# Kernel optimization log

Measured on AMD Instinct MI355X. Metric: run time of the kernel, lower is better.

## Reference

```python
import jax, jax.numpy as jnp
import numpy as np
from jax import lax

HIDDEN = 512
EPS = 1e-5


def _conv(x, w):
    # NCHW conv, 3x3, SAME padding, no bias (padding = kernel_size // 2 == 1)
    return lax.conv_general_dilated(
        x, w, window_strides=(1, 1), padding='SAME',
        dimension_numbers=('NCHW', 'OIHW', 'NCHW'))


def setup_inputs() -> dict:
    key = jax.random.key(0)
    ks = jax.random.split(key, 5)
    N, C, H, W = 32, HIDDEN, 32, 32
    fan = C * 9
    std = float(1.0 / np.sqrt(fan))
    return {
        'x': jax.random.normal(ks[0], (N, C, H, W), jnp.float32),
        'w_q': jax.random.normal(ks[1], (C, C, 3, 3), jnp.float32) * std,
        'w_k': jax.random.normal(ks[2], (C, C, 3, 3), jnp.float32) * std,
        'w_v': jax.random.normal(ks[3], (C, C, 3, 3), jnp.float32) * std,
        'w_o': jax.random.normal(ks[4], (C, C, 3, 3), jnp.float32) * std,
        'gamma': jnp.ones((C,), jnp.float32),
        'beta': jnp.zeros((C,), jnp.float32),
    }


def reference(x, w_q, w_k, w_v, w_o, gamma, beta):
    C = x.shape[1]
    q = _conv(x, w_q)  # [N,C,H,W]
    k = _conv(x, w_k)
    v = _conv(x, w_v)
    # (query.unsqueeze(1) * key.unsqueeze(0)).sum(2) == channel contraction
    att = jnp.einsum('ichw,jchw->ijhw', q, k) / jnp.sqrt(jnp.asarray(C, x.dtype))
    att = jax.nn.softmax(att, axis=1)  # softmax over key instances
    virt = jnp.einsum('ijhw,jchw->ichw', att, v)  # [N,C,H,W]
    # GroupNorm(1, C): normalize over (C,H,W) per instance, per-channel affine
    mean = jnp.mean(virt, axis=(1, 2, 3), keepdims=True)
    var = jnp.var(virt, axis=(1, 2, 3), keepdims=True)
    virt = (virt - mean) * lax.rsqrt(var + EPS)
    virt = virt * gamma[None, :, None, None] + beta[None, :, None, None]
    virt = jax.nn.relu(virt)
    virt = _conv(virt, w_o)
    # Dropout(0.2) is identity in eval mode
    return x + virt
```

## Files before the change

kernel.cpp:

```cpp
#include <hip/hip_runtime.h>

namespace {

constexpr int kN  = 32;
constexpr int kC  = 512;
constexpr int kH  = 32;
constexpr int kW  = 32;
constexpr int kHW = kH * kW;

constexpr int PCH   = 36992;
constexpr size_t WTF_ELEMS = (size_t)9 * kC * kC;
constexpr size_t XH_ELEMS  = (size_t)kN * 16 * PCH;
constexpr size_t QKV_ELEMS = (size_t)kN * kHW * kC;

using bf16x8 = __attribute__((ext_vector_type(8))) short;
using bf16x4 = __attribute__((ext_vector_type(4))) short;
using f32x4  = __attribute__((ext_vector_type(4))) float;

__device__ __forceinline__ float bf2f(short s) {
  unsigned u = ((unsigned)(unsigned short)s) << 16;
  return __builtin_bit_cast(float, u);
}
__device__ __forceinline__ short f2bf(float f) {
  unsigned u = __builtin_bit_cast(unsigned, f);
  u += 0x7FFFu + ((u >> 16) & 1u);
  return (short)(u >> 16);
}
__device__ __forceinline__ void gload_lds16(const void* g, void* l) {
  __builtin_amdgcn_global_load_lds(
      (const __attribute__((address_space(1))) void*)g,
      (__attribute__((address_space(3))) void*)l, 16, 0, 0);
}

__global__ __launch_bounds__(256) void wtf_pack_kernel(
    const float* __restrict__ w, short* __restrict__ wtf) {
  __shared__ float tile[32][289];
  const int co0 = blockIdx.x * 32;
  const int ci0 = blockIdx.y * 32;
  for (int idx = threadIdx.x; idx < 32 * 288; idx += 256) {
    int c = idx % 288, r = idx / 288;
    tile[r][c] = w[(size_t)(co0 + r) * (kC * 9) + (size_t)ci0 * 9 + c];
  }
  __syncthreads();
  const int kkb  = ci0 >> 5;
  const int nnG0 = co0 >> 4;
  for (int g = threadIdx.x; g < 9 * 2 * 64; g += 256) {
    int laneg = g & 63;
    int nnL   = (g >> 6) & 1;
    int t     = g >> 7;
    int hi    = laneg >> 4;
    int coL   = nnL * 16 + (laneg & 15);
    bf16x8 pk;
#pragma unroll
    for (int j = 0; j < 8; ++j) pk[j] = f2bf(tile[coL][(hi * 8 + j) * 9 + t]);
    *(bf16x8*)&wtf[(((size_t)t * 16 + kkb) * 32 + nnG0 + nnL) * 512 + laneg * 8] = pk;
  }
}

__global__ __launch_bounds__(256) void x2xh_kernel(
    const float* __restrict__ x, short* __restrict__ xh) {
  __shared__ float tile[32][33];
  const int ch = blockIdx.x;
  const int h  = blockIdx.y;
  const int n  = blockIdx.z;
  const int w0 = threadIdx.x & 31;
  const int c0 = threadIdx.x >> 5;
#pragma unroll
  for (int pass = 0; pass < 4; ++pass) {
    int cir = pass * 8 + c0;
    tile[w0][cir] = x[(((size_t)n * kC + ch * 32 + cir) * kH + h) * kW + w0];
  }
  __syncthreads();
  const int wv = threadIdx.x >> 3;
  const int g4 = (threadIdx.x & 7) * 4;
  bf16x4 pk;
#pragma unroll
  for (int j = 0; j < 4; ++j) pk[j] = f2bf(tile[wv][g4 + j]);
  *(bf16x4*)&xh[(((size_t)n * 16 + ch) * 1156 + (size_t)(h + 1) * 34 + (wv + 1)) * 32 + g4] = pk;
}

__global__ __launch_bounds__(256, 2) void conv_qkv_kernel(
    const short* __restrict__ xin,
    const short* __restrict__ wtq, const short* __restrict__ wtk,
    const short* __restrict__ wtv,
    short* __restrict__ outq, short* __restrict__ outk,
    short* __restrict__ outv) {
  __shared__ __align__(16) short As[3][8192];
  const int tid  = threadIdx.x;
  const int lane = tid & 63;
  const int l15  = lane & 15, lhi = lane >> 4;
  const int wv   = tid >> 6;
  const int wm   = wv >> 1, wn = wv & 1;
  const int wbase = tid & 192;

  const int xcd = blockIdx.x & 7;
  const int m   = blockIdx.x >> 3;
  const int co0 = (m >> 5) * 64;
  const int spt = m & 7;
  const int n   = xcd * 4 + ((m >> 3) & 3);
  const int h0  = spt * 4;
  const int sp0 = spt * 128;

  const short* srcA = xin + (size_t)n * (16 * PCH) + (size_t)h0 * (34 * 32);
  const size_t boff = ((size_t)(co0 >> 4) + wn * 2) * 512 + lane * 8;
  const short* bp[3] = {wtq + boff, wtk + boff, wtv + boff};

  f32x4 acc[3][4][2];
#pragma unroll
  for (int c = 0; c < 3; ++c)
#pragma unroll
    for (int mf = 0; mf < 4; ++mf)
#pragma unroll
      for (int nf = 0; nf < 2; ++nf)
#pragma unroll
        for (int r = 0; r < 4; ++r) acc[c][mf][nf][r] = 0.f;

#define STAGE_A(kk, buf)                                                      \
  {                                                                           \
    const short* gA = srcA + (size_t)(kk) * PCH;                              \
    _Pragma("unroll") for (int pass = 0; pass < 4; ++pass)                    \
        gload_lds16(gA + (size_t)(pass * 256 + tid) * 8,                      \
                    &As[buf][(pass * 256 + wbase) * 8]);                      \
  }

  STAGE_A(0, 0);
  STAGE_A(1, 1);
  bf16x8 cur[6], nxt[6];
#pragma unroll
  for (int j = 0; j < 6; ++j)
    cur[j] = *(const bf16x8*)&bp[j >> 1][(size_t)(j & 1) * 512];

  int ab = 0;
  int sb = 2;
  for (int kk = 0; kk < 16; ++kk) {
    asm volatile("s_waitcnt vmcnt(10)" ::: "memory");
    __builtin_amdgcn_s_barrier();
#pragma unroll
    for (int t = 0; t < 9; ++t) {
      {
        const int nt  = (t < 8) ? (t + 1) : 0;
        const int nkk = (t < 8) ? kk : kk + 1;
        const size_t bo = (size_t)(nt * 16 + nkk) * 16384;
#pragma unroll
        for (int j = 0; j < 6; ++j)
          nxt[j] = *(const bf16x8*)&bp[j >> 1][bo + (size_t)(j & 1) * 512];
      }
      if (t == 1 && kk < 14) STAGE_A(kk + 2, sb);
      const int dy = t / 3, dx = t % 3;
      bf16x8 a[4];
#pragma unroll
      for (int mf = 0; mf < 4; ++mf) {
        const int pb = (wm * 2 + (mf >> 1) + dy) * 34 + (mf & 1) * 16 + l15 + dx;
        a[mf] = *(const bf16x8*)&As[ab][pb * 32 + lhi * 8];
      }
      __builtin_amdgcn_s_setprio(1);
#pragma unroll
      for (int c = 0; c < 3; ++c)
#pragma unroll
        for (int mf = 0; mf < 4; ++mf)
#pragma unroll
          for (int nf = 0; nf < 2; ++nf)
            acc[c][mf][nf] = __builtin_amdgcn_mfma_f32_16x16x32_bf16(
                a[mf], cur[c * 2 + nf], acc[c][mf][nf], 0, 0, 0);
      __builtin_amdgcn_s_setprio(0);
#pragma unroll
      for (int j = 0; j < 6; ++j) cur[j] = nxt[j];
    }
    ab = (ab == 2) ? 0 : ab + 1;
    sb = (sb == 2) ? 0 : sb + 1;
  }
#undef STAGE_A

  short* outs[3] = {outq, outk, outv};
#pragma unroll
  for (int c = 0; c < 3; ++c) {
    short* out = outs[c];
#pragma unroll
    for (int mf = 0; mf < 4; ++mf)
#pragma unroll
      for (int r = 0; r < 4; ++r) {
        size_t off = ((size_t)n * kHW + sp0 + wm * 64 + mf * 16 + lhi * 4 + r) * kC
                     + co0 + wn * 32 + l15;
#pragma unroll
        for (int nf = 0; nf < 2; ++nf) out[off + nf * 16] = f2bf(acc[c][mf][nf][r]);
      }
  }
}

__global__ __launch_bounds__(256, 3) void conv_o_kernel(
    const short* __restrict__ xin, const short* __restrict__ wtf,
    const float* __restrict__ xres, float* __restrict__ out) {
  __shared__ __align__(16) short As[3][8192];
  const int tid  = threadIdx.x;
  const int lane = tid & 63;
  const int l15  = lane & 15, lhi = lane >> 4;
  const int wv   = tid >> 6;
  const int wm   = wv >> 1, wn = wv & 1;
  const int wbase = tid & 192;

  const int xcd = blockIdx.x & 7;
  const int m   = blockIdx.x >> 3;
  const int co0 = (m >> 5) * 128;
  const int spt = m & 7;
  const int n   = xcd * 4 + ((m >> 3) & 3);
  const int h0  = spt * 4;
  const int sp0 = spt * 128;

  const short* srcA = xin + (size_t)n * (16 * PCH) + (size_t)h0 * (34 * 32);
  const short* bptr = wtf + ((size_t)(co0 >> 4) + wn * 4) * 512 + lane * 8;

  f32x4 acc[4][4];
#pragma unroll
  for (int mf = 0; mf < 4; ++mf)
#pragma unroll
    for (int nf = 0; nf < 4; ++nf)
#pragma unroll
      for (int r = 0; r < 4; ++r) acc[mf][nf][r] = 0.f;

#define STAGE_A(kk, buf)                                                      \
  {                                                                           \
    const short* gA = srcA + (size_t)(kk) * PCH;                              \
    _Pragma("unroll") for (int pass = 0; pass < 4; ++pass)                    \
        gload_lds16(gA + (size_t)(pass * 256 + tid) * 8,                      \
                    &As[buf][(pass * 256 + wbase) * 8]);                      \
  }

  STAGE_A(0, 0);
  STAGE_A(1, 1);
  bf16x8 cur[4], nxt[4];
#pragma unroll
  for (int j = 0; j < 4; ++j)
    cur[j] = *(const bf16x8*)&bptr[(size_t)j * 512];

  int ab = 0, sb = 2;
  for (int kk = 0; kk < 16; ++kk) {
    asm volatile("s_waitcnt vmcnt(8)" ::: "memory");
    __builtin_amdgcn_s_barrier();
#pragma unroll
    for (int t = 0; t < 9; ++t) {
      {
        const int nt  = (t < 8) ? (t + 1) : 0;
        const int nkk = (t < 8) ? kk : kk + 1;
        const size_t bo = (size_t)(nt * 16 + nkk) * 16384;
#pragma unroll
        for (int j = 0; j < 4; ++j)
          nxt[j] = *(const bf16x8*)&bptr[bo + (size_t)j * 512];
      }
      if (t == 1 && kk < 14) STAGE_A(kk + 2, sb);
      const int dy = t / 3, dx = t % 3;
      bf16x8 a[4];
#pragma unroll
      for (int mf = 0; mf < 4; ++mf) {
        const int pb = (wm * 2 + (mf >> 1) + dy) * 34 + (mf & 1) * 16 + l15 + dx;
        a[mf] = *(const bf16x8*)&As[ab][pb * 32 + lhi * 8];
      }
      __builtin_amdgcn_s_setprio(1);
#pragma unroll
      for (int mf = 0; mf < 4; ++mf)
#pragma unroll
        for (int nf = 0; nf < 4; ++nf)
          acc[mf][nf] = __builtin_amdgcn_mfma_f32_16x16x32_bf16(
              a[mf], cur[nf], acc[mf][nf], 0, 0, 0);
      __builtin_amdgcn_s_setprio(0);
#pragma unroll
      for (int j = 0; j < 4; ++j) cur[j] = nxt[j];
    }
    ab = (ab == 2) ? 0 : ab + 1;
    sb = (sb == 2) ? 0 : sb + 1;
  }
#undef STAGE_A

  float* T = (float*)&As[0][0];
#pragma unroll
  for (int nf = 0; nf < 4; ++nf) {
    __syncthreads();
    const int coL = wn * 16 + l15;
#pragma unroll
    for (int mf = 0; mf < 4; ++mf)
#pragma unroll
      for (int r = 0; r < 4; ++r)
        T[coL * 129 + wm * 64 + mf * 16 + lhi * 4 + r] = acc[mf][nf][r];
    __syncthreads();
#pragma unroll
    for (int it = 0; it < 16; ++it) {
      int idx = it * 256 + tid;
      int c = idx >> 7, sp = idx & 127;
      int co = co0 + (c >> 4) * 64 + nf * 16 + (c & 15);
      size_t off = ((size_t)n * kC + co) * kHW + sp0 + sp;
      out[off] = T[c * 129 + sp] + xres[off];
    }
  }
}

__global__ __launch_bounds__(256) void attn_kernel(
    const short* q, const short* __restrict__ k,
    const short* __restrict__ v, short* virt) {
  __shared__ float Qs[32 * 66];
  __shared__ float Ks[32 * 66];
  __shared__ float Ps[32 * 36];
  const int p = blockIdx.x;
  const int tid = threadIdx.x;
  const int i  = tid >> 3;
  const int j0 = (tid & 7) * 4;
  float acc[4] = {0.f, 0.f, 0.f, 0.f};

  for (int c0 = 0; c0 < kC; c0 += 64) {
    __syncthreads();
    {
      int r = tid >> 3, c8 = (tid & 7) * 8;
      size_t g = ((size_t)r * kHW + p) * kC + c0 + c8;
      bf16x8 vq = *(const bf16x8*)&q[g];
      bf16x8 vk = *(const bf16x8*)&k[g];
#pragma unroll
      for (int jj = 0; jj < 8; ++jj) {
        Qs[r * 66 + c8 + jj] = bf2f(vq[jj]);
        Ks[r * 66 + c8 + jj] = bf2f(vk[jj]);
      }
    }
    __syncthreads();
#pragma unroll
    for (int c = 0; c < 64; ++c) {
      float qa = Qs[i * 66 + c];
      acc[0] = fmaf(qa, Ks[(j0 + 0) * 66 + c], acc[0]);
      acc[1] = fmaf(qa, Ks[(j0 + 1) * 66 + c], acc[1]);
      acc[2] = fmaf(qa, Ks[(j0 + 2) * 66 + c], acc[2]);
      acc[3] = fmaf(qa, Ks[(j0 + 3) * 66 + c], acc[3]);
    }
  }
  constexpr float scale = 0.044194173824159216f;
#pragma unroll
  for (int jj = 0; jj < 4; ++jj) acc[jj] *= scale;
  float m = fmaxf(fmaxf(acc[0], acc[1]), fmaxf(acc[2], acc[3]));
  for (int off = 1; off < 8; off <<= 1) m = fmaxf(m, __shfl_xor(m, off));
  float e[4];
  float s = 0.f;
#pragma unroll
  for (int jj = 0; jj < 4; ++jj) {
    e[jj] = __expf(acc[jj] - m);
    s += e[jj];
  }
  for (int off = 1; off < 8; off <<= 1) s += __shfl_xor(s, off);
  const float inv = 1.f / s;
#pragma unroll
  for (int jj = 0; jj < 4; ++jj) Ps[i * 36 + j0 + jj] = e[jj] * inv;

  const int c_ = tid & 63;
  const int i4 = tid >> 6;
  for (int c0 = 0; c0 < kC; c0 += 64) {
    __syncthreads();
    {
      int r = tid >> 3, c8 = (tid & 7) * 8;
      bf16x8 vv = *(const bf16x8*)&v[((size_t)r * kHW + p) * kC + c0 + c8];
#pragma unroll
      for (int jj = 0; jj < 8; ++jj) Qs[r * 66 + c8 + jj] = bf2f(vv[jj]);
    }
    __syncthreads();
#pragma unroll
    for (int it = 0; it < 8; ++it) {
      const int ii = i4 + it * 4;
      float o = 0.f;
#pragma unroll
      for (int j = 0; j < 32; ++j)
        o = fmaf(Ps[ii * 36 + j], Qs[j * 66 + c_], o);
      virt[((size_t)ii * kHW + p) * kC + c0 + c_] = f2bf(o);
    }
  }
}

__global__ __launch_bounds__(256) void gn_part_kernel(
    const short* __restrict__ virt, float* __restrict__ part) {
  const int i   = blockIdx.x >> 3;
  const int seg = blockIdx.x & 7;
  const short* src = virt + (size_t)i * kHW * kC + (size_t)seg * (kHW * kC / 8);
  float s = 0.f, sq = 0.f;
  for (int idx = threadIdx.x; idx < kHW * kC / 8 / 8; idx += 256) {
    bf16x8 vv = *(const bf16x8*)&src[(size_t)idx * 8];
#pragma unroll
    for (int jj = 0; jj < 8; ++jj) {
      float f = bf2f(vv[jj]);
      s += f;
      sq = fmaf(f, f, sq);
    }
  }
  __shared__ float rs[4], rq[4];
  for (int off = 1; off < 64; off <<= 1) {
    s += __shfl_xor(s, off);
    sq += __shfl_xor(sq, off);
  }
  const int lane = threadIdx.x & 63;
  const int wid = threadIdx.x >> 6;
  if (lane == 0) { rs[wid] = s; rq[wid] = sq; }
  __syncthreads();
  if (threadIdx.x == 0) {
    part[blockIdx.x]       = rs[0] + rs[1] + rs[2] + rs[3];
    part[256 + blockIdx.x] = rq[0] + rq[1] + rq[2] + rq[3];
  }
}

__global__ __launch_bounds__(64) void gn_final_kernel(
    const float* __restrict__ part, float* __restrict__ stats) {
  if (threadIdx.x < 32) {
    float s = 0.f, sq = 0.f;
#pragma unroll
    for (int k = 0; k < 8; ++k) {
      s  += part[threadIdx.x * 8 + k];
      sq += part[256 + threadIdx.x * 8 + k];
    }
    constexpr float invn = 1.f / ((float)kHW * kC);
    float mean = s * invn;
    float var = sq * invn - mean * mean;
    stats[threadIdx.x] = mean;
    stats[32 + threadIdx.x] = rsqrtf(var + 1e-5f);
  }
}

__global__ __launch_bounds__(256) void gn_apply_kernel(
    const short* __restrict__ virt, const float* __restrict__ stats,
    const float* __restrict__ gamma, const float* __restrict__ beta,
    short* __restrict__ vh) {
  const size_t g = (size_t)blockIdx.x * 256 + threadIdx.x;
  const int i    = (int)(g >> 16);
  const int rest = (int)(g & 65535);
  const int p    = rest >> 6;
  const int c8g  = rest & 63;
  const int ci   = c8g * 8;
  const float mean = stats[i];
  const float rstd = stats[32 + i];
  bf16x8 vv = *(const bf16x8*)&virt[((size_t)i * kHW + p) * kC + ci];
  const float4 ga = ((const float4*)gamma)[c8g * 2];
  const float4 gb = ((const float4*)gamma)[c8g * 2 + 1];
  const float4 ba = ((const float4*)beta)[c8g * 2];
  const float4 bb = ((const float4*)beta)[c8g * 2 + 1];
  const float gv[8] = {ga.x, ga.y, ga.z, ga.w, gb.x, gb.y, gb.z, gb.w};
  const float bv[8] = {ba.x, ba.y, ba.z, ba.w, bb.x, bb.y, bb.z, bb.w};
  bf16x8 o;
#pragma unroll
  for (int jj = 0; jj < 8; ++jj) {
    float f = (bf2f(vv[jj]) - mean) * rstd;
    f = fmaxf(fmaf(f, gv[jj], bv[jj]), 0.f);
    o[jj] = f2bf(f);
  }
  const size_t dst =
      (((size_t)i * 16 + (ci >> 5)) * 1156 + (size_t)((p >> 5) + 1) * 34 + (p & 31) + 1) * 32
      + (ci & 31);
  *(bf16x8*)&vh[dst] = o;
}

}

extern "C" void kernel_launch(void* const* d_in, const int* in_sizes, int n_in,
                              void* d_out, int out_size, void* d_ws,
                              size_t ws_size, hipStream_t stream) {
  const float* x     = (const float*)d_in[0];
  const float* w_q   = (const float*)d_in[1];
  const float* w_k   = (const float*)d_in[2];
  const float* w_v   = (const float*)d_in[3];
  const float* w_o   = (const float*)d_in[4];
  const float* gamma = (const float*)d_in[5];
  const float* beta  = (const float*)d_in[6];

  short* ws    = (short*)d_ws;
  short* wtf_q = ws;
  short* wtf_k = wtf_q + WTF_ELEMS;
  short* wtf_v = wtf_k + WTF_ELEMS;
  short* wtf_o = wtf_v + WTF_ELEMS;
  short* xh    = wtf_o + WTF_ELEMS;
  short* vh    = xh + XH_ELEMS;
  short* qb    = vh + XH_ELEMS;
  short* kb    = qb + QKV_ELEMS;
  short* vb    = kb + QKV_ELEMS;
  float* stats = (float*)(vb + QKV_ELEMS);
  float* part  = stats + 64;
  short* virt  = qb;
  hipMemsetAsync(xh, 0, (size_t)2 * XH_ELEMS * sizeof(short), stream);

  dim3 wg(16, 16);
  wtf_pack_kernel<<<wg, 256, 0, stream>>>(w_q, wtf_q);
  wtf_pack_kernel<<<wg, 256, 0, stream>>>(w_k, wtf_k);
  wtf_pack_kernel<<<wg, 256, 0, stream>>>(w_v, wtf_v);
  wtf_pack_kernel<<<wg, 256, 0, stream>>>(w_o, wtf_o);

  x2xh_kernel<<<dim3(16, 32, 32), 256, 0, stream>>>(x, xh);

  conv_qkv_kernel<<<2048, 256, 0, stream>>>(xh, wtf_q, wtf_k, wtf_v,
                                            qb, kb, vb);

  attn_kernel<<<kHW, 256, 0, stream>>>(qb, kb, vb, virt);

  gn_part_kernel<<<256, 256, 0, stream>>>(virt, part);
  gn_final_kernel<<<1, 64, 0, stream>>>(part, stats);
  gn_apply_kernel<<<(int)(QKV_ELEMS / 8 / 256), 256, 0, stream>>>(
      virt, stats, gamma, beta, vh);

  conv_o_kernel<<<1024, 256, 0, stream>>>(vh, wtf_o, x, (float*)d_out);
}
```

Before: 658.7 us.

## Use bf16 MFMA for attention score and value products

Rewrites the per-pixel attention kernel so that QK^T and P·V run on 16x16x32 bf16 MFMA instructions instead of scalar fp32 FMAs. Q and K are kept in LDS as bf16 with no conversion, V is transposed into a swizzled LDS tile, and the softmax probabilities are rounded to bf16 before the second product. This cuts ALU and LDS traffic in the attention stage but lowers the precision of the probabilities. The attention kernel is a modest share of total time next to the convolutions.

```diff
diff --git a/kernel.cpp b/kernel.cpp
--- a/kernel.cpp
+++ b/kernel.cpp
@@ -292,77 +292,102 @@
   }
 }
 
-__global__ __launch_bounds__(256) void attn_kernel(
+__global__ __launch_bounds__(256) void attn_mfma_kernel(
     const short* q, const short* __restrict__ k,
     const short* __restrict__ v, short* virt) {
-  __shared__ float Qs[32 * 66];
-  __shared__ float Ks[32 * 66];
-  __shared__ float Ps[32 * 36];
-  const int p = blockIdx.x;
-  const int tid = threadIdx.x;
-  const int i  = tid >> 3;
-  const int j0 = (tid & 7) * 4;
-  float acc[4] = {0.f, 0.f, 0.f, 0.f};
-
+  __shared__ __align__(16) short Qs[32 * 72];
+  __shared__ __align__(16) short Ks[32 * 72];
+  __shared__ __align__(16) float Ps[32 * 36];
+  __shared__ __align__(16) short Vt[64 * 40];
+  const int p    = blockIdx.x;
+  const int tid  = threadIdx.x;
+  const int lane = tid & 63;
+  const int l15  = lane & 15, lhi = lane >> 4;
+  const int w    = tid >> 6;
+  const int iq   = w >> 1, jq = w & 1;
+
+  f32x4 accS = {0.f, 0.f, 0.f, 0.f};
+  const int si = tid >> 3;
+  const int sc = (tid & 7) * 8;
   for (int c0 = 0; c0 < kC; c0 += 64) {
     __syncthreads();
     {
-      int r = tid >> 3, c8 = (tid & 7) * 8;
-      size_t g = ((size_t)r * kHW + p) * kC + c0 + c8;
-      bf16x8 vq = *(const bf16x8*)&q[g];
-      bf16x8 vk = *(const bf16x8*)&k[g];
-#pragma unroll
-      for (int jj = 0; jj < 8; ++jj) {
-        Qs[r * 66 + c8 + jj] = bf2f(vq[jj]);
-        Ks[r * 66 + c8 + jj] = bf2f(vk[jj]);
-      }
+      size_t g = ((size_t)si * kHW + p) * kC + c0 + sc;
+      *(bf16x8*)&Qs[si * 72 + sc] = *(const bf16x8*)&q[g];
+      *(bf16x8*)&Ks[si * 72 + sc] = *(const bf16x8*)&k[g];
     }
     __syncthreads();
 #pragma unroll
-    for (int c = 0; c < 64; ++c) {
-      float qa = Qs[i * 66 + c];
-      acc[0] = fmaf(qa, Ks[(j0 + 0) * 66 + c], acc[0]);
-      acc[1] = fmaf(qa, Ks[(j0 + 1) * 66 + c], acc[1]);
-      acc[2] = fmaf(qa, Ks[(j0 + 2) * 66 + c], acc[2]);
-      acc[3] = fmaf(qa, Ks[(j0 + 3) * 66 + c], acc[3]);
-    }
-  }
+    for (int cs = 0; cs < 2; ++cs) {
+      bf16x8 aq = *(const bf16x8*)&Qs[(iq * 16 + l15) * 72 + cs * 32 + lhi * 8];
+      bf16x8 bk = *(const bf16x8*)&Ks[(jq * 16 + l15) * 72 + cs * 32 + lhi * 8];
+      accS = __builtin_amdgcn_mfma_f32_16x16x32_bf16(aq, bk, accS, 0, 0, 0);
+    }
+  }
+  __syncthreads();
   constexpr float scale = 0.044194173824159216f;
 #pragma unroll
-  for (int jj = 0; jj < 4; ++jj) acc[jj] *= scale;
-  float m = fmaxf(fmaxf(acc[0], acc[1]), fmaxf(acc[2], acc[3]));
-  for (int off = 1; off < 8; off <<= 1) m = fmaxf(m, __shfl_xor(m, off));
-  float e[4];
-  float s = 0.f;
-#pragma unroll
-  for (int jj = 0; jj < 4; ++jj) {
-    e[jj] = __expf(acc[jj] - m);
-    s += e[jj];
-  }
-  for (int off = 1; off < 8; off <<= 1) s += __shfl_xor(s, off);
-  const float inv = 1.f / s;
-#pragma unroll
-  for (int jj = 0; jj < 4; ++jj) Ps[i * 36 + j0 + jj] = e[jj] * inv;
-
-  const int c_ = tid & 63;
-  const int i4 = tid >> 6;
+  for (int r = 0; r < 4; ++r)
+    Ps[(iq * 16 + lhi * 4 + r) * 36 + jq * 16 + l15] = accS[r] * scale;
+  __syncthreads();
+
+  {
+    const int i  = tid >> 3;
+    const int j0 = (tid & 7) * 4;
+    float a0 = Ps[i * 36 + j0], a1 = Ps[i * 36 + j0 + 1];
+    float a2 = Ps[i * 36 + j0 + 2], a3 = Ps[i * 36 + j0 + 3];
+    float mx = fmaxf(fmaxf(a0, a1), fmaxf(a2, a3));
+    for (int off = 1; off < 8; off <<= 1) mx = fmaxf(mx, __shfl_xor(mx, off));
+    float e0 = __expf(a0 - mx), e1 = __expf(a1 - mx);
+    float e2 = __expf(a2 - mx), e3 = __expf(a3 - mx);
+    float s = e0 + e1 + e2 + e3;
+    for (int off = 1; off < 8; off <<= 1) s += __shfl_xor(s, off);
+    const float inv = 1.f / s;
+    Ps[i * 36 + j0]     = e0 * inv;
+    Ps[i * 36 + j0 + 1] = e1 * inv;
+    Ps[i * 36 + j0 + 2] = e2 * inv;
+    Ps[i * 36 + j0 + 3] = e3 * inv;
+  }
+  __syncthreads();
+
+  bf16x8 ap[2];
+#pragma unroll
+  for (int it = 0; it < 2; ++it) {
+    const float* pr = &Ps[(it * 16 + l15) * 36 + lhi * 8];
+    float4 lo = *(const float4*)pr;
+    float4 hi4 = *(const float4*)(pr + 4);
+    ap[it][0] = f2bf(lo.x);  ap[it][1] = f2bf(lo.y);
+    ap[it][2] = f2bf(lo.z);  ap[it][3] = f2bf(lo.w);
+    ap[it][4] = f2bf(hi4.x); ap[it][5] = f2bf(hi4.y);
+    ap[it][6] = f2bf(hi4.z); ap[it][7] = f2bf(hi4.w);
+  }
+
+  const f32x4 zacc = {0.f, 0.f, 0.f, 0.f};
   for (int c0 = 0; c0 < kC; c0 += 64) {
     __syncthreads();
     {
-      int r = tid >> 3, c8 = (tid & 7) * 8;
-      bf16x8 vv = *(const bf16x8*)&v[((size_t)r * kHW + p) * kC + c0 + c8];
-#pragma unroll
-      for (int jj = 0; jj < 8; ++jj) Qs[r * 66 + c8 + jj] = bf2f(vv[jj]);
+      const int j = tid >> 3, c8g = tid & 7;
+      bf16x8 vvv = *(const bf16x8*)&v[((size_t)j * kHW + p) * kC + c0 + c8g * 8];
+#pragma unroll
+      for (int jj = 0; jj < 8; ++jj) {
+        int c = c8g * 8 + jj;
+        int byte = (c * 80 + j * 2) ^ (((c >> 3) & 7) << 4);
+        *(short*)((char*)Vt + byte) = vvv[jj];
+      }
     }
     __syncthreads();
-#pragma unroll
-    for (int it = 0; it < 8; ++it) {
-      const int ii = i4 + it * 4;
-      float o = 0.f;
-#pragma unroll
-      for (int j = 0; j < 32; ++j)
-        o = fmaf(Ps[ii * 36 + j], Qs[j * 66 + c_], o);
-      virt[((size_t)ii * kHW + p) * kC + c0 + c_] = f2bf(o);
+    {
+      const int c = w * 16 + l15;
+      const int byte = (c * 80 + lhi * 16) ^ (((c >> 3) & 7) << 4);
+      bf16x8 bv = *(const bf16x8*)((const char*)Vt + byte);
+#pragma unroll
+      for (int it = 0; it < 2; ++it) {
+        f32x4 o = __builtin_amdgcn_mfma_f32_16x16x32_bf16(ap[it], bv, zacc, 0, 0, 0);
+#pragma unroll
+        for (int r = 0; r < 4; ++r)
+          virt[((size_t)(it * 16 + lhi * 4 + r) * kHW + p) * kC + c0 + w * 16 + l15] =
+              f2bf(o[r]);
+      }
     }
   }
 }
@@ -402,9 +427,9 @@
   if (threadIdx.x < 32) {
     float s = 0.f, sq = 0.f;
 #pragma unroll
-    for (int k = 0; k < 8; ++k) {
-      s  += part[threadIdx.x * 8 + k];
-      sq += part[256 + threadIdx.x * 8 + k];
+    for (int kq = 0; kq < 8; ++kq) {
+      s  += part[threadIdx.x * 8 + kq];
+      sq += part[256 + threadIdx.x * 8 + kq];
     }
     constexpr float invn = 1.f / ((float)kHW * kC);
     float mean = s * invn;
@@ -485,7 +510,7 @@
   conv_qkv_kernel<<<2048, 256, 0, stream>>>(xh, wtf_q, wtf_k, wtf_v,
                                             qb, kb, vb);
 
-  attn_kernel<<<kHW, 256, 0, stream>>>(qb, kb, vb, virt);
+  attn_mfma_kernel<<<kHW, 256, 0, stream>>>(qb, kb, vb, virt);
 
   gn_part_kernel<<<256, 256, 0, stream>>>(virt, part);
   gn_final_kernel<<<1, 64, 0, stream>>>(part, stats);
```

Measured after the change: 586.5 us. -11.0%, faster.
